# Kernel optimization log

Measured on AMD Instinct MI355X. Metric: run time of the kernel, lower is better.

## Reference

```python
import jax, jax.numpy as jnp
import numpy as np

EPS = 1e-7
NUM_NODES = 50000


def setup_inputs() -> dict:
    key = jax.random.key(0)
    k1, k2, k3 = jax.random.split(key, 3)
    n_nodes, n_edges, d = NUM_NODES, 800000, 64
    x = jax.random.normal(k1, (n_nodes, d), dtype=jnp.float32)
    edge_index = jax.random.randint(k2, (2, n_edges), 0, n_nodes, dtype=jnp.int64)
    W = jax.random.normal(k3, (d, d), dtype=jnp.float32) * (1.0 / np.sqrt(d))
    b = jnp.zeros((d,), dtype=jnp.float32)
    beta = jnp.ones((1,), dtype=jnp.float32)
    return {"x": x, "edge_index": edge_index, "W": W, "b": b, "beta": beta}


def _segment_softmax(logits, seg, num_segments):
    # numerically stable softmax over edges grouped by destination node, per channel
    m = jax.ops.segment_max(logits, seg, num_segments=num_segments)  # [N, d]
    m = jnp.where(jnp.isfinite(m), m, 0.0)  # empty segments -> -inf; neutralize
    e = jnp.exp(logits - m[seg])                                      # [E, d]
    denom = jax.ops.segment_sum(e, seg, num_segments=num_segments)    # [N, d]
    return e / (denom[seg] + 1e-16)


def reference(x, edge_index, W, b, beta):
    num_nodes, dim = x.shape
    dst = edge_index[0]
    src = edge_index[1]
    # gather + message encoder (ReLU) + eps
    edge_msg = jax.nn.relu(x[src]) + EPS                               # [E, d]
    # softmax_sg: softmax(beta * msg) per destination segment, beta is a stop-grad scalar
    alpha = _segment_softmax(beta[0] * edge_msg, dst, num_nodes)       # [E, d]
    h = edge_msg * alpha                                               # [E, d]
    # scatter-add aggregation to destination nodes
    agg = jax.ops.segment_sum(h, dst, num_segments=num_nodes)          # [N, d]
    # final dense linear (nn.Linear): agg @ W.T + b
    return agg @ W.T + b
```

## Files before the change

kernel.cpp:

```cpp
#include <hip/hip_runtime.h>
#include <hip/hip_fp16.h>

#define EPS 1e-7f

__global__ void binprep_kernel(const int* __restrict__ dst,
                               const int* __restrict__ src, int E, int cap,
                               const float* __restrict__ x, int M,
                               int* __restrict__ ccur,
                               unsigned* __restrict__ packed,
                               unsigned short* __restrict__ tm,
                               int binBlocks) {
    if ((int)blockIdx.x < binBlocks) {
        __shared__ int lc[256];
        __shared__ int lbase[256];
        int tid = threadIdx.x;
        lc[tid] = 0;
        __syncthreads();
        int e0 = blockIdx.x * 4096;
        int bb[16], rr[16];
        unsigned pk[16];
        #pragma unroll
        for (int i = 0; i < 16; ++i) {
            int e = e0 + i * 256 + tid;
            bb[i] = 0; rr[i] = 0; pk[i] = 0;
            if (e < E) {
                int d = dst[e];
                bb[i] = d >> 8;
                pk[i] = ((unsigned)(d & 255) << 16) | (unsigned)src[e];
                rr[i] = atomicAdd(&lc[bb[i]], 1);
            }
        }
        __syncthreads();
        int c = lc[tid];
        if (c) lbase[tid] = tid * cap + atomicAdd(&ccur[tid], c);
        __syncthreads();
        #pragma unroll
        for (int i = 0; i < 16; ++i) {
            int e = e0 + i * 256 + tid;
            if (e < E) packed[lbase[bb[i]] + rr[i]] = pk[i];
        }
    } else {
        int blk = blockIdx.x - binBlocks;
        int tid = threadIdx.x;
        const unsigned short sent = __half_as_ushort(__float2half_rn(-32.f));
        #pragma unroll
        for (int p = 0; p < 4; ++p) {
            int i = blk * 4096 + p * 1024 + tid * 4;
            if (i < M) {
                float4 v = *(const float4*)&x[i];
                ushort4 o;
                o.x = __half_as_ushort(__float2half_rn(fmaxf(v.x, 0.f) + EPS));
                o.y = __half_as_ushort(__float2half_rn(fmaxf(v.y, 0.f) + EPS));
                o.z = __half_as_ushort(__float2half_rn(fmaxf(v.z, 0.f) + EPS));
                o.w = __half_as_ushort(__float2half_rn(fmaxf(v.w, 0.f) + EPS));
                *(ushort4*)&tm[i] = o;
            } else if (i < M + 64) {
                ushort4 o; o.x = o.y = o.z = o.w = sent;
                *(ushort4*)&tm[i] = o;
            }
        }
    }
}

__global__ void fine_kernel(const unsigned* __restrict__ packed,
                            const int* __restrict__ ccur, int cap,
                            int2* __restrict__ nse,
                            unsigned short* __restrict__ sorted_src, int N) {
    __shared__ int lc[256];
    __shared__ int lcur[256];
    __shared__ int wsum[4];
    __shared__ unsigned stage_pk[6656];
    __shared__ unsigned short stage16[6656];
    int tid = threadIdx.x, b = blockIdx.x;
    int rs = b * cap;
    int len = ccur[b];
    lc[tid] = 0;
    __syncthreads();
    for (int i = tid; i < len; i += 256) {
        unsigned u = packed[rs + i];
        stage_pk[i] = u;
        atomicAdd(&lc[u >> 16], 1);
    }
    __syncthreads();
    int lane = tid & 63, wid = tid >> 6;
    int v = lc[tid];
    int incl = v;
    #pragma unroll
    for (int d = 1; d < 64; d <<= 1) {
        int t = __shfl_up(incl, d, 64);
        if (lane >= d) incl += t;
    }
    if (lane == 63) wsum[wid] = incl;
    __syncthreads();
    int base = 0;
    for (int w = 0; w < wid; ++w) base += wsum[w];
    int excl = base + incl - v;
    lcur[tid] = excl;
    int node = b * 256 + tid;
    if (node < N) nse[node] = make_int2(rs + excl, rs + excl + v);
    __syncthreads();
    for (int i = tid; i < len; i += 256) {
        unsigned u = stage_pk[i];
        int pos = atomicAdd(&lcur[u >> 16], 1);
        stage16[pos] = (unsigned short)(u & 0xffffu);
    }
    __syncthreads();
    unsigned* dst32 = (unsigned*)&sorted_src[rs];
    int len2 = (len + 1) >> 1;
    for (int i = tid; i < len2; i += 256) {
        unsigned lo = stage16[2 * i];
        unsigned hi = (2 * i + 1 < len) ? (unsigned)stage16[2 * i + 1] : 0u;
        dst32[i] = lo | (hi << 16);
    }
}

__device__ __forceinline__ void acc2(unsigned w, float bt,
                                     float& s1a, float& s2a,
                                     float& s1b, float& s2b) {
    float m0 = __half2float(__ushort_as_half((unsigned short)(w & 0xffffu)));
    float m1 = __half2float(__ushort_as_half((unsigned short)(w >> 16)));
    float e0 = __expf(bt * m0);
    float e1 = __expf(bt * m1);
    s1a += e0; s2a = fmaf(m0, e0, s2a);
    s1b += e1; s2b = fmaf(m1, e1, s2b);
}

__launch_bounds__(256)
__global__ void node_kernel(const unsigned short* __restrict__ tm,
                            const int2* __restrict__ nse,
                            const unsigned short* __restrict__ sorted_src,
                            const float* __restrict__ W,
                            const float* __restrict__ b,
                            const float* __restrict__ beta,
                            float* __restrict__ out, int N) {
    __shared__ float WtS[64 * 65];
    __shared__ float aggS[256];

    int tid = threadIdx.x;
    for (int idx = tid * 4; idx < 64 * 64; idx += 256 * 4) {
        float4 w4 = *(const float4*)&W[idx];
        int j = idx >> 6, c = idx & 63;
        WtS[(c + 0) * 65 + j] = w4.x;
        WtS[(c + 1) * 65 + j] = w4.y;
        WtS[(c + 2) * 65 + j] = w4.z;
        WtS[(c + 3) * 65 + j] = w4.w;
    }
    __syncthreads();

    const float bt = beta[0];
    const int wave = tid >> 6;
    const int lane = tid & 63;
    const int quarter = lane >> 4;
    const int chb = (lane & 15) << 3;
    const float bias = b[lane];
    const int stride = gridDim.x * 4;
    const int sent_row = N << 7;
    const unsigned char* tmb = (const unsigned char*)tm;
    float* as = &aggS[wave * 64];

    for (int node = blockIdx.x * 4 + wave; node < N; node += stride) {
        int2 se = nse[node];
        int start = se.x, end = se.y;
        float s1c0 = 0.f, s1c1 = 0.f, s1c2 = 0.f, s1c3 = 0.f;
        float s2c0 = 0.f, s2c1 = 0.f, s2c2 = 0.f, s2c3 = 0.f;
        for (int bse = start; bse < end; bse += 64) {
            int cnt = end - bse;
            if (cnt > 64) cnt = 64;
            int row = (lane < cnt) ? ((int)sorted_src[bse + lane] << 7)
                                   : sent_row;
            for (int k = 0; k < cnt; k += 8) {
                int r0 = __shfl(row, k + quarter, 64);
                int r1 = __shfl(row, k + 4 + quarter, 64);
                uint2 u0 = *(const uint2*)(tmb + (r0 + chb));
                uint2 u1 = *(const uint2*)(tmb + (r1 + chb));
                acc2(u0.x, bt, s1c0, s2c0, s1c1, s2c1);
                acc2(u0.y, bt, s1c2, s2c2, s1c3, s2c3);
                acc2(u1.x, bt, s1c0, s2c0, s1c1, s2c1);
                acc2(u1.y, bt, s1c2, s2c2, s1c3, s2c3);
            }
        }
        #define RED(s) s += __shfl_xor(s, 16, 64); s += __shfl_xor(s, 32, 64)
        RED(s1c0); RED(s1c1); RED(s1c2); RED(s1c3);
        RED(s2c0); RED(s2c1); RED(s2c2); RED(s2c3);
        #undef RED
        float4 g;
        g.x = s2c0 / (s1c0 + 1e-16f);
        g.y = s2c1 / (s1c1 + 1e-16f);
        g.z = s2c2 / (s1c2 + 1e-16f);
        g.w = s2c3 / (s1c3 + 1e-16f);
        if (lane < 16) *(float4*)&as[(lane & 15) << 2] = g;
        float acc = bias;
        #pragma unroll
        for (int c = 0; c < 64; c += 4) {
            float4 a4 = *(const float4*)&as[c];
            acc = fmaf(a4.x, WtS[(c + 0) * 65 + lane], acc);
            acc = fmaf(a4.y, WtS[(c + 1) * 65 + lane], acc);
            acc = fmaf(a4.z, WtS[(c + 2) * 65 + lane], acc);
            acc = fmaf(a4.w, WtS[(c + 3) * 65 + lane], acc);
        }
        out[(size_t)node * 64 + lane] = acc;
    }
}

extern "C" void kernel_launch(void* const* d_in, const int* in_sizes, int n_in,
                              void* d_out, int out_size, void* d_ws, size_t ws_size,
                              hipStream_t stream) {
    const float* x    = (const float*)d_in[0];
    const int*   ei   = (const int*)d_in[1];
    const float* W    = (const float*)d_in[2];
    const float* b    = (const float*)d_in[3];
    const float* beta = (const float*)d_in[4];
    float* out = (float*)d_out;

    const int N = in_sizes[0] / 64;
    const int E = in_sizes[1] / 2;
    const int* dst = ei;
    const int* src = ei + E;
    const int NB = (N + 255) >> 8;
    const int M = N * 64;

    int cap = (E + NB - 1) / NB;
    cap = ((cap + cap / 2 + 256) + 255) & ~255;
    if (cap > 6656) cap = 6656;

    auto align = [](size_t v) { return (v + 255) & ~(size_t)255; };
    size_t off = 0;
    char* ws = (char*)d_ws;
    int2* nse   = (int2*)(ws + off);      off += align((size_t)N * 8);
    int* ccur   = (int*)(ws + off);       off += align((size_t)NB * 4);
    unsigned* packed = (unsigned*)(ws + off);
    off += align((size_t)NB * cap * 4);
    unsigned short* sorted_src = (unsigned short*)(ws + off);
    off += align((size_t)NB * cap * 2);
    unsigned short* tm = (unsigned short*)(ws + off);

    const int binBlocks  = (E + 4095) / 4096;
    const int prepBlocks = (M + 64 + 4095) / 4096;
    hipMemsetAsync(ccur, 0, (size_t)NB * 4, stream);
    binprep_kernel<<<binBlocks + prepBlocks, 256, 0, stream>>>(
        dst, src, E, cap, x, M, ccur, packed, tm, binBlocks);
    fine_kernel<<<NB, 256, 0, stream>>>(packed, ccur, cap, nse, sorted_src, N);

    int node_blocks = (N + 3) / 4;
    if (node_blocks > 2048) node_blocks = 2048;
    node_kernel<<<node_blocks, 256, 0, stream>>>(tm, nse, sorted_src,
                                                 W, b, beta, out, N);
}
```

Before: 136.5 us.

## Double block size to 512 threads and software-prefetch gathers in node kernel

All three kernels move to 512-thread blocks: binning uses smaller per-block edge chunks, the prep path and fine sort stride over 512 threads, and node_kernel handles eight nodes per block. The node gather loop is software-pipelined so the next group of rows is loaded before the current one is accumulated, hiding gather latency. The final softmax ratio uses a fast division intrinsic. Smaller bin chunks mean more global atomics on bin counters, and the prefetch raises register pressure.

```diff
diff --git a/kernel.cpp b/kernel.cpp
--- a/kernel.cpp
+++ b/kernel.cpp
@@ -3,25 +3,26 @@
 
 #define EPS 1e-7f
 
-__global__ void binprep_kernel(const int* __restrict__ dst,
-                               const int* __restrict__ src, int E, int cap,
-                               const float* __restrict__ x, int M,
-                               int* __restrict__ ccur,
-                               unsigned* __restrict__ packed,
-                               unsigned short* __restrict__ tm,
-                               int binBlocks) {
+__global__ __launch_bounds__(512)
+void binprep_kernel(const int* __restrict__ dst,
+                    const int* __restrict__ src, int E, int cap,
+                    const float* __restrict__ x, int M,
+                    int* __restrict__ ccur,
+                    unsigned* __restrict__ packed,
+                    unsigned short* __restrict__ tm,
+                    int binBlocks) {
     if ((int)blockIdx.x < binBlocks) {
         __shared__ int lc[256];
         __shared__ int lbase[256];
         int tid = threadIdx.x;
-        lc[tid] = 0;
+        if (tid < 256) lc[tid] = 0;
         __syncthreads();
-        int e0 = blockIdx.x * 4096;
-        int bb[16], rr[16];
-        unsigned pk[16];
-        #pragma unroll
-        for (int i = 0; i < 16; ++i) {
-            int e = e0 + i * 256 + tid;
+        int e0 = blockIdx.x * 2048;
+        int bb[4], rr[4];
+        unsigned pk[4];
+        #pragma unroll
+        for (int i = 0; i < 4; ++i) {
+            int e = e0 + i * 512 + tid;
             bb[i] = 0; rr[i] = 0; pk[i] = 0;
             if (e < E) {
                 int d = dst[e];
@@ -31,12 +32,14 @@
             }
         }
         __syncthreads();
-        int c = lc[tid];
-        if (c) lbase[tid] = tid * cap + atomicAdd(&ccur[tid], c);
+        if (tid < 256) {
+            int c = lc[tid];
+            if (c) lbase[tid] = tid * cap + atomicAdd(&ccur[tid], c);
+        }
         __syncthreads();
         #pragma unroll
-        for (int i = 0; i < 16; ++i) {
-            int e = e0 + i * 256 + tid;
+        for (int i = 0; i < 4; ++i) {
+            int e = e0 + i * 512 + tid;
             if (e < E) packed[lbase[bb[i]] + rr[i]] = pk[i];
         }
     } else {
@@ -45,7 +48,7 @@
         const unsigned short sent = __half_as_ushort(__float2half_rn(-32.f));
         #pragma unroll
         for (int p = 0; p < 4; ++p) {
-            int i = blk * 4096 + p * 1024 + tid * 4;
+            int i = blk * 8192 + p * 2048 + tid * 4;
             if (i < M) {
                 float4 v = *(const float4*)&x[i];
                 ushort4 o;
@@ -62,10 +65,11 @@
     }
 }
 
-__global__ void fine_kernel(const unsigned* __restrict__ packed,
-                            const int* __restrict__ ccur, int cap,
-                            int2* __restrict__ nse,
-                            unsigned short* __restrict__ sorted_src, int N) {
+__global__ __launch_bounds__(512)
+void fine_kernel(const unsigned* __restrict__ packed,
+                 const int* __restrict__ ccur, int cap,
+                 int2* __restrict__ nse,
+                 unsigned short* __restrict__ sorted_src, int N) {
     __shared__ int lc[256];
     __shared__ int lcur[256];
     __shared__ int wsum[4];
@@ -74,32 +78,38 @@
     int tid = threadIdx.x, b = blockIdx.x;
     int rs = b * cap;
     int len = ccur[b];
-    lc[tid] = 0;
-    __syncthreads();
-    for (int i = tid; i < len; i += 256) {
+    if (tid < 256) lc[tid] = 0;
+    __syncthreads();
+    for (int i = tid; i < len; i += 512) {
         unsigned u = packed[rs + i];
         stage_pk[i] = u;
         atomicAdd(&lc[u >> 16], 1);
     }
     __syncthreads();
-    int lane = tid & 63, wid = tid >> 6;
-    int v = lc[tid];
-    int incl = v;
-    #pragma unroll
-    for (int d = 1; d < 64; d <<= 1) {
-        int t = __shfl_up(incl, d, 64);
-        if (lane >= d) incl += t;
-    }
-    if (lane == 63) wsum[wid] = incl;
-    __syncthreads();
-    int base = 0;
-    for (int w = 0; w < wid; ++w) base += wsum[w];
-    int excl = base + incl - v;
-    lcur[tid] = excl;
-    int node = b * 256 + tid;
-    if (node < N) nse[node] = make_int2(rs + excl, rs + excl + v);
-    __syncthreads();
-    for (int i = tid; i < len; i += 256) {
+    if (tid < 256) {
+        int lane = tid & 63, wid = tid >> 6;
+        int incl = lc[tid];
+        #pragma unroll
+        for (int d = 1; d < 64; d <<= 1) {
+            int t = __shfl_up(incl, d, 64);
+            if (lane >= d) incl += t;
+        }
+        lcur[tid] = incl;
+        if (lane == 63) wsum[wid] = incl;
+    }
+    __syncthreads();
+    if (tid < 256) {
+        int wid = tid >> 6;
+        int base = 0;
+        for (int w = 0; w < wid; ++w) base += wsum[w];
+        int v = lc[tid];
+        int excl = base + lcur[tid] - v;
+        lcur[tid] = excl;
+        int node = b * 256 + tid;
+        if (node < N) nse[node] = make_int2(rs + excl, rs + excl + v);
+    }
+    __syncthreads();
+    for (int i = tid; i < len; i += 512) {
         unsigned u = stage_pk[i];
         int pos = atomicAdd(&lcur[u >> 16], 1);
         stage16[pos] = (unsigned short)(u & 0xffffu);
@@ -107,7 +117,7 @@
     __syncthreads();
     unsigned* dst32 = (unsigned*)&sorted_src[rs];
     int len2 = (len + 1) >> 1;
-    for (int i = tid; i < len2; i += 256) {
+    for (int i = tid; i < len2; i += 512) {
         unsigned lo = stage16[2 * i];
         unsigned hi = (2 * i + 1 < len) ? (unsigned)stage16[2 * i + 1] : 0u;
         dst32[i] = lo | (hi << 16);
@@ -125,19 +135,20 @@
     s1b += e1; s2b = fmaf(m1, e1, s2b);
 }
 
-__launch_bounds__(256)
-__global__ void node_kernel(const unsigned short* __restrict__ tm,
-                            const int2* __restrict__ nse,
-                            const unsigned short* __restrict__ sorted_src,
-                            const float* __restrict__ W,
-                            const float* __restrict__ b,
-                            const float* __restrict__ beta,
-                            float* __restrict__ out, int N) {
+__global__ __launch_bounds__(512)
+void node_kernel(const unsigned short* __restrict__ tm,
+                 const int2* __restrict__ nse,
+                 const unsigned short* __restrict__ sorted_src,
+                 const float* __restrict__ W,
+                 const float* __restrict__ b,
+                 const float* __restrict__ beta,
+                 float* __restrict__ out, int N) {
     __shared__ float WtS[64 * 65];
-    __shared__ float aggS[256];
+    __shared__ float aggS[512];
 
     int tid = threadIdx.x;
-    for (int idx = tid * 4; idx < 64 * 64; idx += 256 * 4) {
+    #pragma unroll
+    for (int idx = tid * 4; idx < 64 * 64; idx += 512 * 4) {
         float4 w4 = *(const float4*)&W[idx];
         int j = idx >> 6, c = idx & 63;
         WtS[(c + 0) * 65 + j] = w4.x;
@@ -153,12 +164,12 @@
     const int quarter = lane >> 4;
     const int chb = (lane & 15) << 3;
     const float bias = b[lane];
-    const int stride = gridDim.x * 4;
+    const int stride = gridDim.x * 8;
     const int sent_row = N << 7;
     const unsigned char* tmb = (const unsigned char*)tm;
     float* as = &aggS[wave * 64];
 
-    for (int node = blockIdx.x * 4 + wave; node < N; node += stride) {
+    for (int node = blockIdx.x * 8 + wave; node < N; node += stride) {
         int2 se = nse[node];
         int start = se.x, end = se.y;
         float s1c0 = 0.f, s1c1 = 0.f, s1c2 = 0.f, s1c3 = 0.f;
@@ -168,26 +179,37 @@
             if (cnt > 64) cnt = 64;
             int row = (lane < cnt) ? ((int)sorted_src[bse + lane] << 7)
                                    : sent_row;
-            for (int k = 0; k < cnt; k += 8) {
-                int r0 = __shfl(row, k + quarter, 64);
-                int r1 = __shfl(row, k + 4 + quarter, 64);
-                uint2 u0 = *(const uint2*)(tmb + (r0 + chb));
-                uint2 u1 = *(const uint2*)(tmb + (r1 + chb));
+            int r0 = __shfl(row, quarter, 64);
+            int r1 = __shfl(row, 4 + quarter, 64);
+            uint2 u0 = *(const uint2*)(tmb + (r0 + chb));
+            uint2 u1 = *(const uint2*)(tmb + (r1 + chb));
+            int k = 0;
+            while (k + 8 < cnt) {
+                int n0 = __shfl(row, k + 8 + quarter, 64);
+                int n1 = __shfl(row, k + 12 + quarter, 64);
+                uint2 v0 = *(const uint2*)(tmb + (n0 + chb));
+                uint2 v1 = *(const uint2*)(tmb + (n1 + chb));
                 acc2(u0.x, bt, s1c0, s2c0, s1c1, s2c1);
                 acc2(u0.y, bt, s1c2, s2c2, s1c3, s2c3);
                 acc2(u1.x, bt, s1c0, s2c0, s1c1, s2c1);
                 acc2(u1.y, bt, s1c2, s2c2, s1c3, s2c3);
+                u0 = v0; u1 = v1;
+                k += 8;
             }
+            acc2(u0.x, bt, s1c0, s2c0, s1c1, s2c1);
+            acc2(u0.y, bt, s1c2, s2c2, s1c3, s2c3);
+            acc2(u1.x, bt, s1c0, s2c0, s1c1, s2c1);
+            acc2(u1.y, bt, s1c2, s2c2, s1c3, s2c3);
         }
         #define RED(s) s += __shfl_xor(s, 16, 64); s += __shfl_xor(s, 32, 64)
         RED(s1c0); RED(s1c1); RED(s1c2); RED(s1c3);
         RED(s2c0); RED(s2c1); RED(s2c2); RED(s2c3);
         #undef RED
         float4 g;
-        g.x = s2c0 / (s1c0 + 1e-16f);
-        g.y = s2c1 / (s1c1 + 1e-16f);
-        g.z = s2c2 / (s1c2 + 1e-16f);
-        g.w = s2c3 / (s1c3 + 1e-16f);
+        g.x = __fdividef(s2c0, s1c0 + 1e-16f);
+        g.y = __fdividef(s2c1, s1c1 + 1e-16f);
+        g.z = __fdividef(s2c2, s1c2 + 1e-16f);
+        g.w = __fdividef(s2c3, s1c3 + 1e-16f);
         if (lane < 16) *(float4*)&as[(lane & 15) << 2] = g;
         float acc = bias;
         #pragma unroll
@@ -234,15 +256,15 @@
     off += align((size_t)NB * cap * 2);
     unsigned short* tm = (unsigned short*)(ws + off);
 
-    const int binBlocks  = (E + 4095) / 4096;
-    const int prepBlocks = (M + 64 + 4095) / 4096;
+    const int binBlocks  = (E + 2047) / 2048;
+    const int prepBlocks = (M + 64 + 8191) / 8192;
     hipMemsetAsync(ccur, 0, (size_t)NB * 4, stream);
-    binprep_kernel<<<binBlocks + prepBlocks, 256, 0, stream>>>(
+    binprep_kernel<<<binBlocks + prepBlocks, 512, 0, stream>>>(
         dst, src, E, cap, x, M, ccur, packed, tm, binBlocks);
-    fine_kernel<<<NB, 256, 0, stream>>>(packed, ccur, cap, nse, sorted_src, N);
-
-    int node_blocks = (N + 3) / 4;
-    if (node_blocks > 2048) node_blocks = 2048;
-    node_kernel<<<node_blocks, 256, 0, stream>>>(tm, nse, sorted_src,
+    fine_kernel<<<NB, 512, 0, stream>>>(packed, ccur, cap, nse, sorted_src, N);
+
+    int node_blocks = (N + 7) / 8;
+    if (node_blocks > 1024) node_blocks = 1024;
+    node_kernel<<<node_blocks, 512, 0, stream>>>(tm, nse, sorted_src,
                                                  W, b, beta, out, N);
 }
```

New measurement: 139.6 us. 1.02x slower.
